# Performance work log

Measured on AMD Instinct MI355X. Metric: run time of the kernel, lower is better.

The kernel has to match this reference:

```python
import jax, jax.numpy as jnp
import numpy as np

B, T, C, H, L, FF, V = 2, 2048, 256, 4, 4, 1024, 32000  # batch, blockSize, embeddingSize, headSize, numLayers, C*linScale, vocabSize


def _layernorm(x, g, b, eps=1e-5):
    m = jnp.mean(x, -1, keepdims=True)
    v = jnp.mean((x - m) ** 2, -1, keepdims=True)
    return (x - m) * jax.lax.rsqrt(v + eps) * g + b


def setup_inputs() -> dict:
    key = jax.random.key(0)
    ks = jax.random.split(key, 12)
    s = 0.02
    rn = lambda k, shape: jax.random.normal(k, shape, jnp.float32) * s
    return {
        "tokens": jax.random.randint(ks[0], (B, T), 0, V),
        "embed": rn(ks[1], (V, C)),
        "pos": rn(ks[2], (T, C)),
        "ln1_g": jnp.ones((L, C)), "ln1_b": jnp.zeros((L, C)),
        "wq": rn(ks[3], (L, H, C, C)),
        "wk": rn(ks[4], (L, H, C, C)),
        "wv": rn(ks[5], (L, H, C, C)),
        "wo": rn(ks[6], (L, H * C, C)), "wo_b": jnp.zeros((L, C)),
        "ln2_g": jnp.ones((L, C)), "ln2_b": jnp.zeros((L, C)),
        "w1": rn(ks[7], (L, C, FF)), "b1": jnp.zeros((L, FF)),
        "w2": rn(ks[8], (L, FF, C)), "b2": jnp.zeros((L, C)),
        "lnf_g": jnp.ones((C,)), "lnf_b": jnp.zeros((C,)),
        "wf": rn(ks[9], (C, V)), "bf": jnp.zeros((V,)),
    }


def reference(tokens, embed, pos, ln1_g, ln1_b, wq, wk, wv, wo, wo_b,
              ln2_g, ln2_b, w1, b1, w2, b2, lnf_g, lnf_b, wf, bf):
    t = tokens.shape[1]
    x = embed[tokens] + pos[:t]                      # [B,T,C]
    scale = 1.0 / np.sqrt(C)                         # np.sqrt(embeddingSize) as in source
    mask = jnp.tril(jnp.ones((t, t), bool))          # True = attend (triu(diag=1) masked)
    for l in range(L):
        # x = LN1(x); x = x + MHSA(x)  (note: LN applied to residual stream itself)
        x = _layernorm(x, ln1_g[l], ln1_b[l])
        q = jnp.einsum('btc,hcd->bhtd', x, wq[l])    # each head uses full C->C projections
        k = jnp.einsum('btc,hcd->bhtd', x, wk[l])
        v = jnp.einsum('btc,hcd->bhtd', x, wv[l])
        scores = jnp.einsum('bhtd,bhsd->bhts', q, k) * scale
        att = jax.nn.softmax(jnp.where(mask, scores, -jnp.inf), axis=-1)
        o = jnp.einsum('bhts,bhsd->bhtd', att, v)
        o = o.transpose(0, 2, 1, 3).reshape(x.shape[0], t, H * C)  # concat heads -> [B,T,H*C]
        x = x + o @ wo[l] + wo_b[l]
        # x = LN2(x); x = x + MLP(x)
        x = _layernorm(x, ln2_g[l], ln2_b[l])
        hdn = jax.nn.relu(x @ w1[l] + b1[l])
        x = x + hdn @ w2[l] + b2[l]
    return _layernorm(x, lnf_g, lnf_b) @ wf + bf     # [B,T,V]
```

## Files before the change

### kernel.cpp

```cpp
#include <hip/hip_runtime.h>
#include <stdint.h>

#define B_ 2
#define T_ 2048
#define C_ 256
#define H_ 4
#define L_ 4
#define FF 1024
#define V_ 32000

typedef short bfrag __attribute__((ext_vector_type(8)));
typedef float facc  __attribute__((ext_vector_type(4)));
typedef short s4v   __attribute__((ext_vector_type(4)));
typedef short s8v   __attribute__((ext_vector_type(8)));
typedef unsigned short u16;

#define FLAG_BIAS 1
#define FLAG_RELU 4
#define FLAG_BF16 8
#define FLAG_NT   16

__device__ __forceinline__ u16 f2bf(float f) {
  uint32_t x = __float_as_uint(f);
  return (u16)((x + 0x7fffu + ((x >> 16) & 1u)) >> 16);
}
__device__ __forceinline__ float bf2f(u16 u) {
  return __uint_as_float(((uint32_t)u) << 16);
}

__device__ __forceinline__ void gload_lds16(const void* g, void* l) {
  __builtin_amdgcn_global_load_lds(
      (const __attribute__((address_space(1))) uint32_t*)g,
      (__attribute__((address_space(3))) uint32_t*)l, 16, 0, 0);
}

__global__ __launch_bounds__(256) void transpose_all(
    const float* __restrict__ wq, const float* __restrict__ wk,
    const float* __restrict__ wv, const float* __restrict__ wo,
    const float* __restrict__ w1, const float* __restrict__ w2,
    const float* __restrict__ wf,
    u16* __restrict__ wqkvT, u16* __restrict__ woT, u16* __restrict__ w1T,
    u16* __restrict__ w2T, u16* __restrict__ wfT) {
  int bid = blockIdx.x;
  const float* in;
  u16* out;
  int R, Cc, cx, ry;
  long long zi, zo;
  if (bid < 3072) {
    int job = bid >> 10, w = bid & 1023;
    int z = w >> 6, t = w & 63;
    cx = t & 7; ry = t >> 3; R = 256; Cc = 256;
    in = (job == 0 ? wq : job == 1 ? wk : wv);
    zi = (long long)z * 65536;
    zo = (long long)(z >> 2) * 786432 + (long long)(z & 3) * 65536
       + (long long)job * 262144;
    out = wqkvT;
  } else if (bid < 4096) {
    int w = bid - 3072; int z = w >> 8, t = w & 255;
    cx = t & 7; ry = t >> 3; R = 1024; Cc = 256;
    in = wo; zi = (long long)z * 262144; zo = zi; out = woT;
  } else if (bid < 5120) {
    int w = bid - 4096; int z = w >> 8, t = w & 255;
    cx = t & 31; ry = t >> 5; R = 256; Cc = 1024;
    in = w1; zi = (long long)z * 262144; zo = zi; out = w1T;
  } else if (bid < 6144) {
    int w = bid - 5120; int z = w >> 8, t = w & 255;
    cx = t & 7; ry = t >> 3; R = 1024; Cc = 256;
    in = w2; zi = (long long)z * 262144; zo = zi; out = w2T;
  } else {
    int t = bid - 6144; cx = t % 1000; ry = t / 1000;
    R = 256; Cc = 32000; in = wf; zi = 0; zo = 0; out = wfT;
  }
  __shared__ float tile[32][33];
  int c0 = cx * 32, r0 = ry * 32;
  int tx = threadIdx.x & 31, ty = threadIdx.x >> 5;
#pragma unroll
  for (int i = ty; i < 32; i += 8)
    tile[i][tx] = in[zi + (long long)(r0 + i) * Cc + (c0 + tx)];
  __syncthreads();
#pragma unroll
  for (int i = ty; i < 32; i += 8)
    out[zo + (long long)(c0 + i) * R + (r0 + tx)] = f2bf(tile[tx][i]);
}

__global__ __launch_bounds__(256) void transpose_v(const u16* __restrict__ qkv,
                                                   u16* __restrict__ vt) {
  __shared__ u16 tile[32][33];
  int z = blockIdx.z, b = z >> 2, h = z & 3;
  const u16* in = qkv + (long long)b * T_ * 3072 + 2048 + h * 256;
  int t0 = blockIdx.x * 32, d0 = blockIdx.y * 32;
  int tx = threadIdx.x & 31, ty = threadIdx.x >> 5;
#pragma unroll
  for (int i = ty; i < 32; i += 8)
    tile[i][tx] = in[(long long)(t0 + i) * 3072 + (d0 + tx)];
  __syncthreads();
#pragma unroll
  for (int i = ty; i < 32; i += 8)
    vt[((long long)z * 256 + d0 + i) * T_ + (t0 + tx)] = tile[tx][i];
}

__global__ __launch_bounds__(256) void embed_ln(const int* __restrict__ tok,
                                                const float* __restrict__ emb,
                                                const float* __restrict__ pos,
                                                u16* __restrict__ xn,
                                                const float* __restrict__ g,
                                                const float* __restrict__ b) {
  int wid = threadIdx.x >> 6, lane = threadIdx.x & 63;
  int row = blockIdx.x * 4 + wid;
  int t = row & (T_ - 1);
  float4 ev = ((const float4*)(emb + (long long)tok[row] * C_))[lane];
  float4 pv = ((const float4*)(pos + (long long)t * C_))[lane];
  float4 v;
  v.x = ev.x + pv.x; v.y = ev.y + pv.y; v.z = ev.z + pv.z; v.w = ev.w + pv.w;
  float s = v.x + v.y + v.z + v.w;
#pragma unroll
  for (int o = 32; o > 0; o >>= 1) s += __shfl_xor(s, o);
  float mean = s * (1.f / 256.f);
  float d0 = v.x - mean, d1 = v.y - mean, d2 = v.z - mean, d3 = v.w - mean;
  float q2 = d0 * d0 + d1 * d1 + d2 * d2 + d3 * d3;
#pragma unroll
  for (int o = 32; o > 0; o >>= 1) q2 += __shfl_xor(q2, o);
  float rstd = rsqrtf(q2 * (1.f / 256.f) + 1e-5f);
  float4 gv = ((const float4*)g)[lane];
  float4 bv = ((const float4*)b)[lane];
  u16 tmp[4] = {f2bf(d0 * rstd * gv.x + bv.x), f2bf(d1 * rstd * gv.y + bv.y),
                f2bf(d2 * rstd * gv.z + bv.z), f2bf(d3 * rstd * gv.w + bv.w)};
  *(s4v*)&xn[(long long)row * C_ + lane * 4] = *(const s4v*)tmp;
}

__global__ __launch_bounds__(256) void reduce_ln(const u16* __restrict__ pbuf,
                                                 u16* __restrict__ xn,
                                                 const float* __restrict__ bias,
                                                 const float* __restrict__ g,
                                                 const float* __restrict__ b) {
  int wid = threadIdx.x >> 6, lane = threadIdx.x & 63;
  long long row = (long long)blockIdx.x * 4 + wid;
  const u16* p = pbuf + row * C_ + lane * 4;
  const int SL = 1048576;
  s4v rv = *(const s4v*)&xn[row * C_ + lane * 4];
  float4 bi = ((const float4*)bias)[lane];
  float4 v;
  v.x = bf2f((u16)rv[0]) + bi.x;
  v.y = bf2f((u16)rv[1]) + bi.y;
  v.z = bf2f((u16)rv[2]) + bi.z;
  v.w = bf2f((u16)rv[3]) + bi.w;
#pragma unroll
  for (int sI = 0; sI < 4; ++sI) {
    s4v pv = *(const s4v*)(p + sI * SL);
    v.x += bf2f((u16)pv[0]);
    v.y += bf2f((u16)pv[1]);
    v.z += bf2f((u16)pv[2]);
    v.w += bf2f((u16)pv[3]);
  }
  float s = v.x + v.y + v.z + v.w;
#pragma unroll
  for (int o = 32; o > 0; o >>= 1) s += __shfl_xor(s, o);
  float mean = s * (1.f / 256.f);
  float d0 = v.x - mean, d1 = v.y - mean, d2 = v.z - mean, d3 = v.w - mean;
  float q2 = d0 * d0 + d1 * d1 + d2 * d2 + d3 * d3;
#pragma unroll
  for (int o = 32; o > 0; o >>= 1) q2 += __shfl_xor(q2, o);
  float rstd = rsqrtf(q2 * (1.f / 256.f) + 1e-5f);
  float4 gv = ((const float4*)g)[lane];
  float4 bv = ((const float4*)b)[lane];
  u16 tmp[4] = {f2bf(d0 * rstd * gv.x + bv.x), f2bf(d1 * rstd * gv.y + bv.y),
                f2bf(d2 * rstd * gv.z + bv.z), f2bf(d3 * rstd * gv.w + bv.w)};
  *(s4v*)&xn[row * C_ + lane * 4] = *(const s4v*)tmp;
}

__global__ __launch_bounds__(256, 1) void flash_k(const u16* __restrict__ qkv,
                                                  const u16* __restrict__ vt,
                                                  u16* __restrict__ ocat) {
  __shared__ u16 Klds[2][64 * 256];
  __shared__ u16 Vlds[2][256 * 64];
  __shared__ u16 Plds[4][1024];
  int ib = blockIdx.x, z = blockIdx.y;
  int b = z >> 2, h = z & 3;
  int lo0 = ib * 32, hi0 = 2016 - ib * 32;
  int tid = threadIdx.x, lane = tid & 63, wid = tid >> 6;
  int l15 = lane & 15, lg = lane >> 4;
  int wrow0 = (wid < 2) ? (lo0 + wid * 16) : (hi0 + (wid - 2) * 16);
  int jmax = (hi0 + 31) >> 6;

  bfrag qf[8];
  {
    const u16* qrow = qkv + (long long)(b * T_ + wrow0 + l15) * 3072 + h * 256 + lg * 8;
#pragma unroll
    for (int ks = 0; ks < 8; ++ks) qf[ks] = *(const bfrag*)(qrow + ks * 32);
  }
  facc zf = {0.f, 0.f, 0.f, 0.f};
  facc O[16];
#pragma unroll
  for (int nb = 0; nb < 16; ++nb) O[nb] = zf;
  float mrow[4] = {-1e30f, -1e30f, -1e30f, -1e30f};
  float lrow[4] = {0.f, 0.f, 0.f, 0.f};

  const u16* kgbase = qkv + (long long)(b * T_) * 3072 + 1024 + h * 256;
  const u16* vgbase = vt + (long long)z * 256 * 2048;

  auto stage = [&](int j) {
    int kv0 = j * 64;
    int bufi = j & 1;
#pragma unroll
    for (int c = 0; c < 8; ++c) {
      int chunk = wid * 8 + c;
      int krow = chunk * 2 + (lane >> 5);
      int kcb = ((lane & 31) * 16) ^ ((krow & 7) << 4);
      gload_lds16(kgbase + (long long)(kv0 + krow) * 3072 + (kcb >> 1),
                  &Klds[bufi][chunk * 512 + lane * 8]);
      int drow = chunk * 8 + (lane >> 3);
      int vcb = ((lane & 7) * 16) ^ ((drow & 7) << 4);
      gload_lds16(vgbase + (long long)drow * 2048 + kv0 + (vcb >> 1),
                  &Vlds[bufi][chunk * 512 + lane * 8]);
    }
  };

  stage(0);
  for (int j = 0; j <= jmax; ++j) {
    __syncthreads();
    if (j < jmax) stage(j + 1);
    const u16* Kb = Klds[j & 1];
    const u16* Vb = Vlds[j & 1];
    int kv0 = j * 64;
    bool skip = (kv0 > wrow0 + 15);
    if (!skip) {
      bool full = (kv0 + 63 <= wrow0);
      facc s[4];
#pragma unroll
      for (int nb = 0; nb < 4; ++nb) {
        s[nb] = zf;
#pragma unroll
        for (int ks = 0; ks < 8; ++ks) {
          int row = nb * 16 + l15;
          bfrag kb = *(const bfrag*)&Kb[row * 256 +
              (((ks * 64 + lg * 16) ^ ((row & 7) << 4)) >> 1)];
          s[nb] = __builtin_amdgcn_mfma_f32_16x16x32_bf16(qf[ks], kb, s[nb], 0, 0, 0);
        }
      }
      float pmax[4] = {-1e30f, -1e30f, -1e30f, -1e30f};
#pragma unroll
      for (int nb = 0; nb < 4; ++nb) {
        int col = kv0 + nb * 16 + l15;
#pragma unroll
        for (int i = 0; i < 4; ++i) {
          float vsc = s[nb][i] * 0.0625f;
          int rowa = wrow0 + lg * 4 + i;
          if (!full && col > rowa) vsc = -1e30f;
          s[nb][i] = vsc;
          pmax[i] = fmaxf(pmax[i], vsc);
        }
      }
#pragma unroll
      for (int i = 0; i < 4; ++i) {
        pmax[i] = fmaxf(pmax[i], __shfl_xor(pmax[i], 1));
        pmax[i] = fmaxf(pmax[i], __shfl_xor(pmax[i], 2));
        pmax[i] = fmaxf(pmax[i], __shfl_xor(pmax[i], 4));
        pmax[i] = fmaxf(pmax[i], __shfl_xor(pmax[i], 8));
      }
      float corr[4], rsum[4];
#pragma unroll
      for (int i = 0; i < 4; ++i) {
        float mn = fmaxf(mrow[i], pmax[i]);
        corr[i] = __expf(mrow[i] - mn);
        mrow[i] = mn;
        rsum[i] = 0.f;
      }
#pragma unroll
      for (int nb = 0; nb < 4; ++nb)
#pragma unroll
        for (int i = 0; i < 4; ++i) {
          float p = __expf(s[nb][i] - mrow[i]);
          s[nb][i] = p;
          rsum[i] += p;
        }
#pragma unroll
      for (int i = 0; i < 4; ++i) {
        rsum[i] += __shfl_xor(rsum[i], 1);
        rsum[i] += __shfl_xor(rsum[i], 2);
        rsum[i] += __shfl_xor(rsum[i], 4);
        rsum[i] += __shfl_xor(rsum[i], 8);
        lrow[i] = lrow[i] * corr[i] + rsum[i];
      }
#pragma unroll
      for (int nb = 0; nb < 16; ++nb)
#pragma unroll
        for (int i = 0; i < 4; ++i) O[nb][i] *= corr[i];
      u16* Pw = (u16*)Plds[wid];
#pragma unroll
      for (int nb = 0; nb < 4; ++nb)
#pragma unroll
        for (int i = 0; i < 4; ++i) {
          int row = lg * 4 + i;
          Pw[(row * 128 + ((nb * 32 + l15 * 2) ^ ((row & 7) << 4))) >> 1] =
              f2bf(s[nb][i]);
        }
      bfrag pa[2];
#pragma unroll
      for (int ksv = 0; ksv < 2; ++ksv)
        pa[ksv] = *(const bfrag*)&Pw[l15 * 64 +
            (((ksv * 64 + lg * 16) ^ ((l15 & 7) << 4)) >> 1)];
#pragma unroll
      for (int nb = 0; nb < 16; ++nb) {
        int d = nb * 16 + l15;
#pragma unroll
        for (int ksv = 0; ksv < 2; ++ksv) {
          bfrag vb = *(const bfrag*)&Vb[d * 64 +
              (((ksv * 64 + lg * 16) ^ ((d & 7) << 4)) >> 1)];
          O[nb] = __builtin_amdgcn_mfma_f32_16x16x32_bf16(pa[ksv], vb, O[nb], 0, 0, 0);
        }
      }
    }
  }
  float rinv[4];
#pragma unroll
  for (int i = 0; i < 4; ++i) rinv[i] = 1.f / lrow[i];
  u16* orow = ocat + (long long)(b * T_ + wrow0) * 1024 + h * 256;
#pragma unroll
  for (int nb = 0; nb < 16; ++nb)
#pragma unroll
    for (int i = 0; i < 4; ++i) {
      int row = lg * 4 + i;
      orow[(long long)row * 1024 + nb * 16 + l15] = f2bf(O[nb][i] * rinv[i]);
    }
}

template <int BM, int BN, int LDOUT, int FLAGS, int SPLITK, int SWAP>
__global__ __launch_bounds__(256) void gemm_nt(
    const u16* __restrict__ A, int lda,
    const u16* __restrict__ B, int ldb,
    int K, void* outp, const float* __restrict__ bias) {
  constexpr int MR = BM / 32, NR = BN / 32;
  __shared__ u16 As[2][BM * 32];
  __shared__ u16 Bs[2][BN * 32];
  int gx = SWAP ? blockIdx.y : blockIdx.x;
  int gy = SWAP ? blockIdx.x : blockIdx.y;
  int z = blockIdx.z;
  const u16* Ab = A + (long long)gy * BM * lda + (SPLITK ? z * 256 : 0);
  const u16* Bb = B + (long long)gx * BN * ldb + (SPLITK ? z * 256 : 0);
  float* outf = (float*)outp + (SPLITK ? (long long)z * 1048576 : 0);
  u16* outh = (u16*)outp + (SPLITK ? (long long)z * 1048576 : 0);
  int tid = threadIdx.x;
  int lane = tid & 63, wid = tid >> 6;
  int wr = (wid >> 1) * (BM / 2), wc = (wid & 1) * (BN / 2);
  int srow = tid >> 2, scol = (tid & 3) * 8;

  auto stage = [&](int t, int bufi) {
    int k0 = t * 32;
#pragma unroll
    for (int i = 0; i < BM / 64; ++i)
      gload_lds16(Ab + (long long)(srow + i * 64) * lda + k0 + scol,
                  &As[bufi][(srow + i * 64) * 32 + scol]);
#pragma unroll
    for (int i = 0; i < BN / 64; ++i)
      gload_lds16(Bb + (long long)(srow + i * 64) * ldb + k0 + scol,
                  &Bs[bufi][(srow + i * 64) * 32 + scol]);
  };

  facc acc[MR][NR];
  facc zf = {0.f, 0.f, 0.f, 0.f};
#pragma unroll
  for (int m = 0; m < MR; ++m)
#pragma unroll
    for (int n = 0; n < NR; ++n) acc[m][n] = zf;

  int nt = K >> 5;
  stage(0, 0);
  __syncthreads();
  for (int t = 0; t < nt; ++t) {
    int cur = t & 1;
    if (t + 1 < nt) stage(t + 1, cur ^ 1);
    int kk = (lane >> 4) * 8;
    int ar = wr + (lane & 15);
    int br = wc + (lane & 15);
    bfrag af[MR], bfv[NR];
#pragma unroll
    for (int m = 0; m < MR; ++m) af[m] = *(const bfrag*)&As[cur][(ar + m * 16) * 32 + kk];
#pragma unroll
    for (int n = 0; n < NR; ++n) bfv[n] = *(const bfrag*)&Bs[cur][(br + n * 16) * 32 + kk];
#pragma unroll
    for (int m = 0; m < MR; ++m)
#pragma unroll
      for (int n = 0; n < NR; ++n)
        acc[m][n] = __builtin_amdgcn_mfma_f32_16x16x32_bf16(af[m], bfv[n], acc[m][n], 0, 0, 0);
    __syncthreads();
  }

  int rg = (lane >> 4) * 4;
  int cl = lane & 15;
  int rbase = gy * BM + wr + rg;
  int cbase = gx * BN + wc + cl;
#pragma unroll
  for (int m = 0; m < MR; ++m) {
#pragma unroll
    for (int n = 0; n < NR; ++n) {
      int c_abs = cbase + n * 16;
      float bvv = (FLAGS & FLAG_BIAS) ? bias[c_abs] : 0.f;
#pragma unroll
      for (int i = 0; i < 4; ++i) {
        int r = rbase + m * 16 + i;
        float val = acc[m][n][i] + bvv;
        if (FLAGS & FLAG_RELU) val = fmaxf(val, 0.f);
        int oi = r * LDOUT + c_abs;
        if (FLAGS & FLAG_BF16) outh[oi] = f2bf(val);
        else if (FLAGS & FLAG_NT) __builtin_nontemporal_store(val, &outf[oi]);
        else outf[oi] = val;
      }
    }
  }
}

extern "C" void kernel_launch(void* const* d_in, const int* in_sizes, int n_in,
                              void* d_out, int out_size, void* d_ws, size_t ws_size,
                              hipStream_t stream) {
  (void)in_sizes; (void)n_in; (void)out_size; (void)ws_size;
  const int*   tokens = (const int*)d_in[0];
  const float* embed  = (const float*)d_in[1];
  const float* pos    = (const float*)d_in[2];
  const float* ln1_g  = (const float*)d_in[3];
  const float* ln1_b  = (const float*)d_in[4];
  const float* wq     = (const float*)d_in[5];
  const float* wk     = (const float*)d_in[6];
  const float* wv     = (const float*)d_in[7];
  const float* wo     = (const float*)d_in[8];
  const float* wo_b   = (const float*)d_in[9];
  const float* ln2_g  = (const float*)d_in[10];
  const float* ln2_b  = (const float*)d_in[11];
  const float* w1     = (const float*)d_in[12];
  const float* b1     = (const float*)d_in[13];
  const float* w2     = (const float*)d_in[14];
  const float* b2     = (const float*)d_in[15];
  const float* lnf_g  = (const float*)d_in[16];
  const float* lnf_b  = (const float*)d_in[17];
  const float* wf     = (const float*)d_in[18];
  const float* bf     = (const float*)d_in[19];
  float* out = (float*)d_out;

  char* ws = (char*)d_ws;
  size_t off = 0;
  auto alloc = [&](size_t bytes) -> char* {
    char* p = ws + off;
    off += (bytes + 255) & ~(size_t)255;
    return p;
  };
  const long long NR = (long long)B_ * T_;
  u16* xn    = (u16*)alloc(NR * C_ * 2);
  u16* qkv   = (u16*)alloc(NR * 3072LL * 2);
  u16* vt    = (u16*)alloc((long long)B_ * H_ * C_ * T_ * 2);
  u16* ocat  = (u16*)alloc(NR * (long long)(H_ * C_) * 2);
  u16* hdn   = (u16*)alloc(NR * (long long)FF * 2);
  u16* pbuf  = (u16*)alloc(4LL * NR * C_ * 2);
  u16* wqkvT = (u16*)alloc((long long)L_ * 3 * H_ * C_ * C_ * 2);
  u16* woT   = (u16*)alloc((long long)L_ * C_ * (H_ * C_) * 2);
  u16* w1T   = (u16*)alloc((long long)L_ * FF * C_ * 2);
  u16* w2T   = (u16*)alloc((long long)L_ * C_ * FF * 2);
  u16* wfT   = (u16*)alloc((long long)V_ * C_ * 2);

  dim3 tb(256);

  transpose_all<<<dim3(14144), tb, 0, stream>>>(wq, wk, wv, wo, w1, w2, wf,
                                                wqkvT, woT, w1T, w2T, wfT);
  embed_ln<<<dim3(1024), tb, 0, stream>>>(tokens, embed, pos, xn, ln1_g, ln1_b);

  for (int l = 0; l < L_; ++l) {
    gemm_nt<64, 64, 3072, FLAG_BF16, 0, 0><<<dim3(48, 64, 1), tb, 0, stream>>>(
        xn, C_, wqkvT + (long long)l * 3 * 1024 * 256, C_, C_, qkv, nullptr);
    transpose_v<<<dim3(64, 8, 8), tb, 0, stream>>>(qkv, vt);
    flash_k<<<dim3(32, 8), tb, 0, stream>>>(qkv, vt, ocat);
    gemm_nt<64, 64, 256, FLAG_BF16, 1, 0><<<dim3(4, 64, 4), tb, 0, stream>>>(
        ocat, H_ * C_, woT + (long long)l * C_ * H_ * C_, H_ * C_, C_, pbuf, nullptr);
    reduce_ln<<<dim3(1024), tb, 0, stream>>>(pbuf, xn, wo_b + l * C_,
                                             ln2_g + l * C_, ln2_b + l * C_);
    gemm_nt<64, 64, 1024, FLAG_BIAS | FLAG_RELU | FLAG_BF16, 0, 0>
        <<<dim3(16, 64, 1), tb, 0, stream>>>(
        xn, C_, w1T + (long long)l * FF * C_, C_, C_, hdn, b1 + l * FF);
    gemm_nt<64, 64, 256, FLAG_BF16, 1, 0><<<dim3(4, 64, 4), tb, 0, stream>>>(
        hdn, FF, w2T + (long long)l * C_ * FF, FF, C_, pbuf, nullptr);
    const float* ng = (l < 3) ? (ln1_g + (l + 1) * C_) : lnf_g;
    const float* nb = (l < 3) ? (ln1_b + (l + 1) * C_) : lnf_b;
    reduce_ln<<<dim3(1024), tb, 0, stream>>>(pbuf, xn, b2 + l * C_, ng, nb);
  }
  gemm_nt<128, 128, 32000, FLAG_BIAS | FLAG_NT, 0, 1><<<dim3(32, 250, 1), tb, 0, stream>>>(
      xn, C_, wfT, C_, C_, out, bf);
}
```

Baseline: 806.6 us.

## Give each flash-attention wave 32 query rows to reuse K/V fragments

The flash attention kernel drops from 4 waves per block to 2, and each wave now processes two 16-row query tiles (32 rows). Each K and V fragment read from LDS then feeds two MFMAs, halving LDS fragment traffic per MFMA, and the two waves split the staging loads between them. The cost is higher register pressure (two O accumulators of 16 fragments each, two sets of Q fragments) and half as many waves per block, so latency hiding across the 256 blocks drops.

```diff
diff --git a/kernel.cpp b/kernel.cpp
--- a/kernel.cpp
+++ b/kernel.cpp
@@ -168,32 +168,38 @@
   *(s4v*)&xn[row * C_ + lane * 4] = *(const s4v*)tmp;
 }
 
-__global__ __launch_bounds__(256, 1) void flash_k(const u16* __restrict__ qkv,
+__global__ __launch_bounds__(128, 1) void flash_k(const u16* __restrict__ qkv,
                                                   const u16* __restrict__ vt,
                                                   u16* __restrict__ ocat) {
   __shared__ u16 Klds[2][64 * 256];
   __shared__ u16 Vlds[2][256 * 64];
-  __shared__ u16 Plds[4][1024];
+  __shared__ u16 Plds[2][2048];
   int ib = blockIdx.x, z = blockIdx.y;
   int b = z >> 2, h = z & 3;
-  int lo0 = ib * 32, hi0 = 2016 - ib * 32;
   int tid = threadIdx.x, lane = tid & 63, wid = tid >> 6;
   int l15 = lane & 15, lg = lane >> 4;
-  int wrow0 = (wid < 2) ? (lo0 + wid * 16) : (hi0 + (wid - 2) * 16);
-  int jmax = (hi0 + 31) >> 6;
-
-  bfrag qf[8];
-  {
-    const u16* qrow = qkv + (long long)(b * T_ + wrow0 + l15) * 3072 + h * 256 + lg * 8;
-#pragma unroll
-    for (int ks = 0; ks < 8; ++ks) qf[ks] = *(const bfrag*)(qrow + ks * 32);
+  int wrow0 = (wid == 0) ? (ib * 32) : (2016 - ib * 32);
+  int jmax = (2016 - ib * 32 + 31) >> 6;
+
+  bfrag qf[2][8];
+#pragma unroll
+  for (int m = 0; m < 2; ++m) {
+    const u16* qrow = qkv + (long long)(b * T_ + wrow0 + m * 16 + l15) * 3072
+                    + h * 256 + lg * 8;
+#pragma unroll
+    for (int ks = 0; ks < 8; ++ks) qf[m][ks] = *(const bfrag*)(qrow + ks * 32);
   }
   facc zf = {0.f, 0.f, 0.f, 0.f};
-  facc O[16];
-#pragma unroll
-  for (int nb = 0; nb < 16; ++nb) O[nb] = zf;
-  float mrow[4] = {-1e30f, -1e30f, -1e30f, -1e30f};
-  float lrow[4] = {0.f, 0.f, 0.f, 0.f};
+  facc O[2][16];
+#pragma unroll
+  for (int m = 0; m < 2; ++m)
+#pragma unroll
+    for (int nb = 0; nb < 16; ++nb) O[m][nb] = zf;
+  float mrow[2][4], lrow[2][4];
+#pragma unroll
+  for (int m = 0; m < 2; ++m)
+#pragma unroll
+    for (int i = 0; i < 4; ++i) { mrow[m][i] = -1e30f; lrow[m][i] = 0.f; }
 
   const u16* kgbase = qkv + (long long)(b * T_) * 3072 + 1024 + h * 256;
   const u16* vgbase = vt + (long long)z * 256 * 2048;
@@ -202,8 +208,8 @@
     int kv0 = j * 64;
     int bufi = j & 1;
 #pragma unroll
-    for (int c = 0; c < 8; ++c) {
-      int chunk = wid * 8 + c;
+    for (int c = 0; c < 16; ++c) {
+      int chunk = wid * 16 + c;
       int krow = chunk * 2 + (lane >> 5);
       int kcb = ((lane & 31) * 16) ^ ((krow & 7) << 4);
       gload_lds16(kgbase + (long long)(kv0 + krow) * 3072 + (kcb >> 1),
@@ -222,83 +228,96 @@
     const u16* Kb = Klds[j & 1];
     const u16* Vb = Vlds[j & 1];
     int kv0 = j * 64;
-    bool skip = (kv0 > wrow0 + 15);
+    bool skip = (kv0 > wrow0 + 31);
     if (!skip) {
       bool full = (kv0 + 63 <= wrow0);
-      facc s[4];
+      facc s[2][4];
+#pragma unroll
+      for (int m = 0; m < 2; ++m)
+#pragma unroll
+        for (int nb = 0; nb < 4; ++nb) s[m][nb] = zf;
 #pragma unroll
       for (int nb = 0; nb < 4; ++nb) {
-        s[nb] = zf;
 #pragma unroll
         for (int ks = 0; ks < 8; ++ks) {
           int row = nb * 16 + l15;
           bfrag kb = *(const bfrag*)&Kb[row * 256 +
               (((ks * 64 + lg * 16) ^ ((row & 7) << 4)) >> 1)];
-          s[nb] = __builtin_amdgcn_mfma_f32_16x16x32_bf16(qf[ks], kb, s[nb], 0, 0, 0);
+#pragma unroll
+          for (int m = 0; m < 2; ++m)
+            s[m][nb] = __builtin_amdgcn_mfma_f32_16x16x32_bf16(qf[m][ks], kb, s[m][nb], 0, 0, 0);
         }
       }
-      float pmax[4] = {-1e30f, -1e30f, -1e30f, -1e30f};
-#pragma unroll
-      for (int nb = 0; nb < 4; ++nb) {
-        int col = kv0 + nb * 16 + l15;
+#pragma unroll
+      for (int m = 0; m < 2; ++m) {
+        float pmax[4] = {-1e30f, -1e30f, -1e30f, -1e30f};
+#pragma unroll
+        for (int nb = 0; nb < 4; ++nb) {
+          int col = kv0 + nb * 16 + l15;
+#pragma unroll
+          for (int i = 0; i < 4; ++i) {
+            float vsc = s[m][nb][i] * 0.0625f;
+            int rowa = wrow0 + m * 16 + lg * 4 + i;
+            if (!full && col > rowa) vsc = -1e30f;
+            s[m][nb][i] = vsc;
+            pmax[i] = fmaxf(pmax[i], vsc);
+          }
+        }
 #pragma unroll
         for (int i = 0; i < 4; ++i) {
-          float vsc = s[nb][i] * 0.0625f;
-          int rowa = wrow0 + lg * 4 + i;
-          if (!full && col > rowa) vsc = -1e30f;
-          s[nb][i] = vsc;
-          pmax[i] = fmaxf(pmax[i], vsc);
-        }
+          pmax[i] = fmaxf(pmax[i], __shfl_xor(pmax[i], 1));
+          pmax[i] = fmaxf(pmax[i], __shfl_xor(pmax[i], 2));
+          pmax[i] = fmaxf(pmax[i], __shfl_xor(pmax[i], 4));
+          pmax[i] = fmaxf(pmax[i], __shfl_xor(pmax[i], 8));
+        }
+        float corr[4], rsum[4];
+#pragma unroll
+        for (int i = 0; i < 4; ++i) {
+          float mn = fmaxf(mrow[m][i], pmax[i]);
+          corr[i] = __expf(mrow[m][i] - mn);
+          mrow[m][i] = mn;
+          rsum[i] = 0.f;
+        }
+#pragma unroll
+        for (int nb = 0; nb < 4; ++nb)
+#pragma unroll
+          for (int i = 0; i < 4; ++i) {
+            float p = __expf(s[m][nb][i] - mrow[m][i]);
+            s[m][nb][i] = p;
+            rsum[i] += p;
+          }
+#pragma unroll
+        for (int i = 0; i < 4; ++i) {
+          rsum[i] += __shfl_xor(rsum[i], 1);
+          rsum[i] += __shfl_xor(rsum[i], 2);
+          rsum[i] += __shfl_xor(rsum[i], 4);
+          rsum[i] += __shfl_xor(rsum[i], 8);
+          lrow[m][i] = lrow[m][i] * corr[i] + rsum[i];
+        }
+#pragma unroll
+        for (int nb = 0; nb < 16; ++nb)
+#pragma unroll
+          for (int i = 0; i < 4; ++i) O[m][nb][i] *= corr[i];
+        u16* Pw = (u16*)Plds[wid];
+#pragma unroll
+        for (int nb = 0; nb < 4; ++nb)
+#pragma unroll
+          for (int i = 0; i < 4; ++i) {
+            int row = m * 16 + lg * 4 + i;
+            Pw[(row * 128 + ((nb * 32 + l15 * 2) ^ ((row & 7) << 4))) >> 1] =
+                f2bf(s[m][nb][i]);
+          }
       }
-#pragma unroll
-      for (int i = 0; i < 4; ++i) {
-        pmax[i] = fmaxf(pmax[i], __shfl_xor(pmax[i], 1));
-        pmax[i] = fmaxf(pmax[i], __shfl_xor(pmax[i], 2));
-        pmax[i] = fmaxf(pmax[i], __shfl_xor(pmax[i], 4));
-        pmax[i] = fmaxf(pmax[i], __shfl_xor(pmax[i], 8));
-      }
-      float corr[4], rsum[4];
-#pragma unroll
-      for (int i = 0; i < 4; ++i) {
-        float mn = fmaxf(mrow[i], pmax[i]);
-        corr[i] = __expf(mrow[i] - mn);
-        mrow[i] = mn;
-        rsum[i] = 0.f;
-      }
-#pragma unroll
-      for (int nb = 0; nb < 4; ++nb)
-#pragma unroll
-        for (int i = 0; i < 4; ++i) {
-          float p = __expf(s[nb][i] - mrow[i]);
-          s[nb][i] = p;
-          rsum[i] += p;
-        }
-#pragma unroll
-      for (int i = 0; i < 4; ++i) {
-        rsum[i] += __shfl_xor(rsum[i], 1);
-        rsum[i] += __shfl_xor(rsum[i], 2);
-        rsum[i] += __shfl_xor(rsum[i], 4);
-        rsum[i] += __shfl_xor(rsum[i], 8);
-        lrow[i] = lrow[i] * corr[i] + rsum[i];
-      }
-#pragma unroll
-      for (int nb = 0; nb < 16; ++nb)
-#pragma unroll
-        for (int i = 0; i < 4; ++i) O[nb][i] *= corr[i];
       u16* Pw = (u16*)Plds[wid];
-#pragma unroll
-      for (int nb = 0; nb < 4; ++nb)
-#pragma unroll
-        for (int i = 0; i < 4; ++i) {
-          int row = lg * 4 + i;
-          Pw[(row * 128 + ((nb * 32 + l15 * 2) ^ ((row & 7) << 4))) >> 1] =
-              f2bf(s[nb][i]);
-        }
-      bfrag pa[2];
-#pragma unroll
-      for (int ksv = 0; ksv < 2; ++ksv)
-        pa[ksv] = *(const bfrag*)&Pw[l15 * 64 +
-            (((ksv * 64 + lg * 16) ^ ((l15 & 7) << 4)) >> 1)];
+      bfrag pa[2][2];
+#pragma unroll
+      for (int m = 0; m < 2; ++m)
+#pragma unroll
+        for (int ksv = 0; ksv < 2; ++ksv) {
+          int prow = m * 16 + l15;
+          pa[m][ksv] = *(const bfrag*)&Pw[prow * 64 +
+              (((ksv * 64 + lg * 16) ^ ((prow & 7) << 4)) >> 1)];
+        }
 #pragma unroll
       for (int nb = 0; nb < 16; ++nb) {
         int d = nb * 16 + l15;
@@ -306,22 +325,27 @@
         for (int ksv = 0; ksv < 2; ++ksv) {
           bfrag vb = *(const bfrag*)&Vb[d * 64 +
               (((ksv * 64 + lg * 16) ^ ((d & 7) << 4)) >> 1)];
-          O[nb] = __builtin_amdgcn_mfma_f32_16x16x32_bf16(pa[ksv], vb, O[nb], 0, 0, 0);
+#pragma unroll
+          for (int m = 0; m < 2; ++m)
+            O[m][nb] = __builtin_amdgcn_mfma_f32_16x16x32_bf16(pa[m][ksv], vb, O[m][nb], 0, 0, 0);
         }
       }
     }
   }
-  float rinv[4];
-#pragma unroll
-  for (int i = 0; i < 4; ++i) rinv[i] = 1.f / lrow[i];
-  u16* orow = ocat + (long long)(b * T_ + wrow0) * 1024 + h * 256;
-#pragma unroll
-  for (int nb = 0; nb < 16; ++nb)
-#pragma unroll
-    for (int i = 0; i < 4; ++i) {
-      int row = lg * 4 + i;
-      orow[(long long)row * 1024 + nb * 16 + l15] = f2bf(O[nb][i] * rinv[i]);
-    }
+#pragma unroll
+  for (int m = 0; m < 2; ++m) {
+    float rinv[4];
+#pragma unroll
+    for (int i = 0; i < 4; ++i) rinv[i] = 1.f / lrow[m][i];
+    u16* orow = ocat + (long long)(b * T_ + wrow0 + m * 16) * 1024 + h * 256;
+#pragma unroll
+    for (int nb = 0; nb < 16; ++nb)
+#pragma unroll
+      for (int i = 0; i < 4; ++i) {
+        int row = lg * 4 + i;
+        orow[(long long)row * 1024 + nb * 16 + l15] = f2bf(O[m][nb][i] * rinv[i]);
+      }
+  }
 }
 
 template <int BM, int BN, int LDOUT, int FLAGS, int SPLITK, int SWAP>
@@ -465,7 +489,7 @@
     gemm_nt<64, 64, 3072, FLAG_BF16, 0, 0><<<dim3(48, 64, 1), tb, 0, stream>>>(
         xn, C_, wqkvT + (long long)l * 3 * 1024 * 256, C_, C_, qkv, nullptr);
     transpose_v<<<dim3(64, 8, 8), tb, 0, stream>>>(qkv, vt);
-    flash_k<<<dim3(32, 8), tb, 0, stream>>>(qkv, vt, ocat);
+    flash_k<<<dim3(32, 8), dim3(128), 0, stream>>>(qkv, vt, ocat);
     gemm_nt<64, 64, 256, FLAG_BF16, 1, 0><<<dim3(4, 64, 4), tb, 0, stream>>>(
         ocat, H_ * C_, woT + (long long)l * C_ * H_ * C_, H_ * C_, C_, pbuf, nullptr);
     reduce_ln<<<dim3(1024), tb, 0, stream>>>(pbuf, xn, wo_b + l * C_,
```

Measured after the change: 1.140 ms. +41.4%, slower.
